# Kernel optimization log

Measured on AMD Instinct MI355X. Metric: run time of the kernel, lower is better.

## Reference

```python
import jax, jax.numpy as jnp
import numpy as np

N, E, IN, OUT = 50000, 1600000, 64, 64
DIM, K = 2, 5          # pseudo-coordinate dim, kernel size per dim
KP = K ** DIM          # 25 kernel weight matrices
S = 2 ** DIM           # 4 non-zero linear B-spline basis products per edge
# bit pattern per basis product: bits[s, d] in {0,1}
_BITS = np.array([[(s >> d) & 1 for d in range(DIM)] for s in range(S)], dtype=np.int32)
_OFFS = np.array([K ** (DIM - 1 - d) for d in range(DIM)], dtype=np.int32)  # row-major flatten


def setup_inputs() -> dict:
    key = jax.random.key(0)
    ks = jax.random.split(key, 6)
    x = jax.random.normal(ks[0], (N, IN), dtype=jnp.float32)
    edge_index = jax.random.randint(ks[1], (2, E), 0, N)
    pseudo = jax.random.uniform(ks[2], (E, DIM), dtype=jnp.float32)
    bnd = 1.0 / np.sqrt(KP * IN)  # matches uniform(size) init in reset_parameters
    weight = jax.random.uniform(ks[3], (KP, IN, OUT), dtype=jnp.float32, minval=-bnd, maxval=bnd)
    root_weight = jax.random.uniform(ks[4], (IN, OUT), dtype=jnp.float32, minval=-bnd, maxval=bnd)
    bias = jax.random.uniform(ks[5], (OUT,), dtype=jnp.float32, minval=-bnd, maxval=bnd)
    return {"x": x, "edge_index": edge_index, "pseudo": pseudo,
            "weight": weight, "root_weight": root_weight, "bias": bias}


def _basis_and_index(pseudo):
    # open B-spline, degree 1: scale by (K - 1)
    v = pseudo * jnp.asarray(K - 1, pseudo.dtype)          # [E, DIM]
    lo = jnp.floor(v)
    frac = v - lo                                          # [E, DIM]
    lo = lo.astype(jnp.int32)
    bits = jnp.asarray(_BITS)                              # [S, DIM]
    # basis[e, s] = prod_d (frac if bit else 1-frac)
    terms = jnp.where(bits[None].astype(bool), frac[:, None, :], 1.0 - frac[:, None, :])
    basis = jnp.prod(terms, axis=-1)                       # [E, S]
    idx_d = (lo[:, None, :] + bits[None]) % K              # [E, S, DIM]; wrap is harmless (basis=0 there)
    idx = jnp.sum(idx_d * jnp.asarray(_OFFS), axis=-1)     # [E, S] flat weight index in [0, KP)
    return basis, idx


def reference(x, edge_index, pseudo, weight, root_weight, bias):
    row, col = edge_index[0], edge_index[1]                # row = target, col = source
    basis, idx = _basis_and_index(pseudo)                  # [E,S], [E,S]
    x_src = x[col]                                         # [E, IN] gather
    # Accumulate basis-weighted source features per (target node, kernel index),
    # then apply the dense [KP, IN, OUT] weights once (same math, no [E,IN,OUT] blowup).
    acc = jnp.zeros((N * KP, IN), x.dtype)
    for s in range(S):  # S=4, fixed structural loop
        acc = acc + jax.ops.segment_sum(basis[:, s:s + 1] * x_src,
                                        row * KP + idx[:, s], num_segments=N * KP)
    out = jnp.einsum('nki,kio->no', acc.reshape(N, KP, IN), weight)  # [N, OUT]
    deg = jax.ops.segment_sum(jnp.ones((E,), x.dtype), row, num_segments=N)
    out = out / jnp.clip(deg, 1.0)[:, None]                # mean over neighbors (1/N(i))
    return out + x @ root_weight + bias
```

## Files before the change

kernel.cpp:

```cpp
#include <hip/hip_runtime.h>
#include <hip/hip_fp16.h>
#include <hip/hip_bf16.h>


#define NN    50000
#define EE    1600000
#define NPB   16
#define KD    1664
#define ASTB  1672
#define CAP   56
#define OFCAP 16384

#define REC_B 6250
#define XB_B  1563
#define WT_B  104

typedef unsigned short ushort_t;
typedef __attribute__((ext_vector_type(8))) short short8;
typedef __attribute__((ext_vector_type(4))) float f32x4;

static __device__ __forceinline__ ushort_t f2bf(float f) {
  union { float f; unsigned u; } v; v.f = f;
  return (ushort_t)((v.u + 0x7fffu + ((v.u >> 16) & 1u)) >> 16);
}
static __device__ __forceinline__ unsigned pk2bf(float a, float b) {
  __hip_bfloat162 h = __float22bfloat162_rn(make_float2(a, b));
  union { __hip_bfloat162 h; unsigned u; } cv; cv.h = h; return cv.u;
}
union S8 { short8 s; unsigned u[4]; };

__global__ __launch_bounds__(256) void k_prep(
    const int* __restrict__ ei, const float* __restrict__ pseudo,
    int* __restrict__ cursor, uint2* __restrict__ recs, uint4* __restrict__ ofl,
    const float* __restrict__ x, ushort_t* __restrict__ xb,
    const float* __restrict__ w, const float* __restrict__ root,
    ushort_t* __restrict__ wt, int useXB) {
  const int b = blockIdx.x;
  if (b < REC_B) {
    int e = b * 256 + threadIdx.x;
    int row = ei[e], col = ei[EE + e];
    float2 pv = ((const float2*)pseudo)[e];
    float v0 = pv.x * 4.0f, v1 = pv.y * 4.0f;
    int slot = atomicAdd(&cursor[row], 1);
    if (slot < CAP) {
      unsigned h0 = __half_as_ushort(__float2half(v0));
      unsigned h1 = __half_as_ushort(__float2half(v1));
      recs[row * CAP + slot] = make_uint2((unsigned)col, h0 | (h1 << 16));
    } else {
      int o = atomicAdd(&cursor[NN], 1);
      if (o < OFCAP)
        ofl[o] = make_uint4((unsigned)row, (unsigned)col,
                            __float_as_uint(v0), __float_as_uint(v1));
    }
  } else if (b < REC_B + XB_B) {
    if (!useXB) return;
    int t = (b - REC_B) * 256 + threadIdx.x;
    if (t < NN * 8) {
      const float4* xp = (const float4*)x + (size_t)t * 2;
      float4 aa = xp[0], bb = xp[1];
      S8 o;
      o.u[0] = pk2bf(aa.x, aa.y); o.u[1] = pk2bf(aa.z, aa.w);
      o.u[2] = pk2bf(bb.x, bb.y); o.u[3] = pk2bf(bb.z, bb.w);
      ((short8*)xb)[t] = o.s;
    }
  } else {
    int t = (b - REC_B - XB_B) * 256 + threadIdx.x;
    int idx = t * 4;
    if (idx < 64 * KD) {
      int o = idx / KD, k = idx - o * KD;
#pragma unroll
      for (int q = 0; q < 4; ++q) {
        int kk = k + q;
        wt[idx + q] = (kk < 1600) ? f2bf(w[kk * 64 + o]) : f2bf(root[(kk - 1600) * 64 + o]);
      }
    }
  }
}

template <bool XBF>
__global__ __launch_bounds__(1024) void k_main(
    const uint2* __restrict__ recs, const int* __restrict__ cursor,
    const uint4* __restrict__ ofl,
    const float* __restrict__ x, const ushort_t* __restrict__ xb,
    const ushort_t* __restrict__ wt, const float* __restrict__ bias,
    float* __restrict__ out) {
  __shared__ ushort_t accS[NPB * ASTB];
  __shared__ float    outp[4 * NPB * 64];
  __shared__ float    sinv[NPB];
  const int tid = threadIdx.x;
  const int lane = tid & 63;
  const int w = tid >> 6;
  const int nb = blockIdx.x * NPB;
  const int node = nb + w;

  const int dg = cursor[node];
  const int m = min(dg, CAP);
  const float dcf = (float)max(dg, 1);
  if (lane == 0) sinv[w] = 1.0f / dcf;
  accS[w * ASTB + 1600 + lane] = f2bf(x[(size_t)node * 64 + lane] * dcf);

  const int m15 = lane & 15, quad = lane >> 4;
  const float r0f = (float)(m15 / 5),        c0f = (float)(m15 % 5);
  const float r1f = (float)((16 + m15) / 5), c1f = (float)((16 + m15) % 5);

  f32x4 acc[2][4];
#pragma unroll
  for (int a = 0; a < 2; ++a)
#pragma unroll
    for (int b = 0; b < 4; ++b) acc[a][b] = (f32x4){0.f, 0.f, 0.f, 0.f};

  const uint2* bket = recs + (size_t)node * CAP;
  unsigned rcx = 0u, rcy = 0x7C007C00u;
  if (lane < m) { uint2 rr = bket[lane]; rcx = rr.x; rcy = rr.y; }

  for (int e0 = 0; e0 < m; e0 += 32) {
    const int eb = e0 + quad * 8;
    unsigned cj[8], pj[8];
#pragma unroll
    for (int j = 0; j < 8; ++j) {
      cj[j] = (unsigned)__shfl((int)rcx, eb + j);
      pj[j] = (unsigned)__shfl((int)rcy, eb + j);
    }
    S8 aT0, aT1, bT[4];
#pragma unroll
    for (int p = 0; p < 4; ++p) {
      if (XBF) {
        const ushort_t* xr0 = xb + (size_t)cj[2 * p] * 64 + m15;
        const ushort_t* xr1 = xb + (size_t)cj[2 * p + 1] * 64 + m15;
        unsigned l0 = xr0[0], l1 = xr0[16], l2 = xr0[32], l3 = xr0[48];
        unsigned h0 = xr1[0], h1 = xr1[16], h2 = xr1[32], h3 = xr1[48];
        bT[0].u[p] = l0 | (h0 << 16);
        bT[1].u[p] = l1 | (h1 << 16);
        bT[2].u[p] = l2 | (h2 << 16);
        bT[3].u[p] = l3 | (h3 << 16);
      } else {
        const float* xr0 = x + (size_t)cj[2 * p] * 64 + m15;
        const float* xr1 = x + (size_t)cj[2 * p + 1] * 64 + m15;
        bT[0].u[p] = pk2bf(xr0[0],  xr1[0]);
        bT[1].u[p] = pk2bf(xr0[16], xr1[16]);
        bT[2].u[p] = pk2bf(xr0[32], xr1[32]);
        bT[3].u[p] = pk2bf(xr0[48], xr1[48]);
      }
    }
#pragma unroll
    for (int p = 0; p < 4; ++p) {
      float a0[2], a1[2];
#pragma unroll
      for (int q = 0; q < 2; ++q) {
        unsigned pv = pj[2 * p + q];
        float v0 = __half2float(__ushort_as_half((ushort_t)(pv & 0xFFFFu)));
        float v1 = __half2float(__ushort_as_half((ushort_t)(pv >> 16)));
        a0[q] = fmaxf(0.f, 1.f - fabsf(v0 - r0f)) * fmaxf(0.f, 1.f - fabsf(v1 - c0f));
        a1[q] = fmaxf(0.f, 1.f - fabsf(v0 - r1f)) * fmaxf(0.f, 1.f - fabsf(v1 - c1f));
      }
      aT0.u[p] = pk2bf(a0[0], a0[1]);
      aT1.u[p] = pk2bf(a1[0], a1[1]);
    }
    __builtin_amdgcn_s_setprio(1);
#pragma unroll
    for (int t = 0; t < 4; ++t) {
      acc[0][t] = __builtin_amdgcn_mfma_f32_16x16x32_bf16(aT0.s, bT[t].s, acc[0][t], 0, 0, 0);
      acc[1][t] = __builtin_amdgcn_mfma_f32_16x16x32_bf16(aT1.s, bT[t].s, acc[1][t], 0, 0, 0);
    }
    __builtin_amdgcn_s_setprio(0);
  }

  {
    int ofc = min(cursor[NN], OFCAP);
    for (int i = 0; i < ofc; ++i) {
      uint4 r = ofl[i];
      if ((int)r.x != node) continue;
      float v0 = __uint_as_float(r.z), v1 = __uint_as_float(r.w);
      float h00 = fmaxf(0.f, 1.f - fabsf(v0 - r0f));
      float h01 = fmaxf(0.f, 1.f - fabsf(v1 - c0f));
      float h10 = fmaxf(0.f, 1.f - fabsf(v0 - r1f));
      float h11 = fmaxf(0.f, 1.f - fabsf(v1 - c1f));
      float mk = (quad == 0) ? 1.0f : 0.0f;
      S8 aT0, aT1, bT[4];
#pragma unroll
      for (int p = 0; p < 4; ++p) { aT0.u[p] = 0; aT1.u[p] = 0; }
      aT0.u[0] = pk2bf(h00 * h01 * mk, 0.0f);
      aT1.u[0] = pk2bf(h10 * h11 * mk, 0.0f);
      const float* xr = x + (size_t)r.y * 64 + m15;
#pragma unroll
      for (int t = 0; t < 4; ++t) {
        float xv = xr[16 * t];
#pragma unroll
        for (int p = 0; p < 4; ++p) bT[t].u[p] = pk2bf(xv, xv);
      }
#pragma unroll
      for (int t = 0; t < 4; ++t) {
        acc[0][t] = __builtin_amdgcn_mfma_f32_16x16x32_bf16(aT0.s, bT[t].s, acc[0][t], 0, 0, 0);
        acc[1][t] = __builtin_amdgcn_mfma_f32_16x16x32_bf16(aT1.s, bT[t].s, acc[1][t], 0, 0, 0);
      }
    }
  }

#pragma unroll
  for (int mt = 0; mt < 2; ++mt)
#pragma unroll
    for (int r = 0; r < 4; ++r) {
      int kp = mt * 16 + quad * 4 + r;
      if (kp < 25) {
#pragma unroll
        for (int nt = 0; nt < 4; ++nt)
          accS[w * ASTB + kp * 64 + nt * 16 + m15] = f2bf(acc[mt][nt][r]);
      }
    }
  __syncthreads();

  {
    const int ntile = w & 3, kh = w >> 2;
    const int m2 = lane & 15, quad2 = lane >> 4;
    const int nn2 = ntile * 16 + m2;
    f32x4 d = {0.0f, 0.0f, 0.0f, 0.0f};
    const ushort_t* ab = &accS[m2 * ASTB + kh * 416 + quad2 * 8];
    const ushort_t* wb = &wt[(size_t)nn2 * KD + kh * 416 + quad2 * 8];
    for (int kk = 0; kk < 13; ++kk) {
      short8 af = *(const short8*)(ab + kk * 32);
      short8 bf = *(const short8*)(wb + kk * 32);
      d = __builtin_amdgcn_mfma_f32_16x16x32_bf16(af, bf, d, 0, 0, 0);
    }
#pragma unroll
    for (int r = 0; r < 4; ++r)
      outp[kh * (NPB * 64) + (quad2 * 4 + r) * 64 + ntile * 16 + m2] = d[r];
  }
  __syncthreads();

  {
    float conv = outp[0 * (NPB * 64) + w * 64 + lane]
               + outp[1 * (NPB * 64) + w * 64 + lane]
               + outp[2 * (NPB * 64) + w * 64 + lane]
               + outp[3 * (NPB * 64) + w * 64 + lane];
    out[(size_t)node * 64 + lane] = conv * sinv[w] + bias[lane];
  }
}

__global__ void k_sentinel(float* __restrict__ out) {
  int i = blockIdx.x * 256 + threadIdx.x;
  if (i < NN * 64) out[i] = 1000.0f;
}

extern "C" void kernel_launch(void* const* d_in, const int* in_sizes, int n_in,
                              void* d_out, int out_size, void* d_ws, size_t ws_size,
                              hipStream_t stream) {
  const float* x      = (const float*)d_in[0];
  const int*   ei     = (const int*)d_in[1];
  const float* pseudo = (const float*)d_in[2];
  const float* w      = (const float*)d_in[3];
  const float* root   = (const float*)d_in[4];
  const float* bias   = (const float*)d_in[5];
  float* out = (float*)d_out;
  (void)in_sizes; (void)n_in; (void)out_size;

  char* ws = (char*)d_ws;
  size_t off = 0;
  auto alloc = [&](size_t bytes) { size_t r = off; off += (bytes + 511) & ~(size_t)511; return r; };
  ushort_t* wt     = (ushort_t*)(ws + alloc((size_t)64 * KD * 2));
  int*      cursor = (int*)(ws + alloc((size_t)(NN + 1) * 4));
  uint4*    ofl    = (uint4*)(ws + alloc((size_t)OFCAP * 16));
  uint2*    recs   = (uint2*)(ws + alloc((size_t)NN * CAP * 8));
  size_t baseNeed  = off;
  ushort_t* xb     = (ushort_t*)(ws + alloc((size_t)NN * 64 * 2));
  size_t fullNeed  = off;

  if (ws_size < baseNeed) {
    k_sentinel<<<(NN * 64 + 255) / 256, 256, 0, stream>>>(out);
    return;
  }
  const int useXB = (ws_size >= fullNeed) ? 1 : 0;

  hipMemsetAsync(cursor, 0, (size_t)(NN + 1) * 4, stream);
  k_prep<<<REC_B + XB_B + WT_B, 256, 0, stream>>>(ei, pseudo, cursor, recs, ofl,
                                                  x, xb, w, root, wt, useXB);
  if (useXB)
    k_main<true><<<NN / NPB, 1024, 0, stream>>>(recs, cursor, ofl, x, xb, wt, bias, out);
  else
    k_main<false><<<NN / NPB, 1024, 0, stream>>>(recs, cursor, ofl, x, xb, wt, bias, out);
}
```

Measured before the change: 352.8 us.

## Replace per-node fixed-capacity buckets with two-level coarse bucket sort into CSR

Edge binning now scatters records into sharded coarse buckets of 128 nodes using few, padded atomic counters. A new sort kernel counts and scans per-node degrees in shared memory and writes a compact CSR layout with per-node start and degree. The main kernel reads variable-length neighbour lists, reloading records every 64 edges, so the overflow list scan over all nodes is gone. Gathers are issued ahead of the basis arithmetic, and launch bounds request more occupancy. This costs an extra kernel launch and another pass over the edges, and coarse buckets that overflow their fixed capacity silently drop edges.

```diff
diff --git a/kernel.cpp b/kernel.cpp
--- a/kernel.cpp
+++ b/kernel.cpp
@@ -8,8 +8,11 @@
 #define NPB   16
 #define KD    1664
 #define ASTB  1672
-#define CAP   56
-#define OFCAP 16384
+
+#define NB    391
+#define NSH   4
+#define CCAP  1280
+#define CSTR  16
 
 #define REC_B 6250
 #define XB_B  1563
@@ -31,30 +34,27 @@
 
 __global__ __launch_bounds__(256) void k_prep(
     const int* __restrict__ ei, const float* __restrict__ pseudo,
-    int* __restrict__ cursor, uint2* __restrict__ recs, uint4* __restrict__ ofl,
+    int* __restrict__ ccur, uint2* __restrict__ coarse,
     const float* __restrict__ x, ushort_t* __restrict__ xb,
     const float* __restrict__ w, const float* __restrict__ root,
     ushort_t* __restrict__ wt, int useXB) {
   const int b = blockIdx.x;
+  const int tid = threadIdx.x;
   if (b < REC_B) {
-    int e = b * 256 + threadIdx.x;
+    int e = b * 256 + tid;
     int row = ei[e], col = ei[EE + e];
     float2 pv = ((const float2*)pseudo)[e];
     float v0 = pv.x * 4.0f, v1 = pv.y * 4.0f;
-    int slot = atomicAdd(&cursor[row], 1);
-    if (slot < CAP) {
-      unsigned h0 = __half_as_ushort(__float2half(v0));
-      unsigned h1 = __half_as_ushort(__float2half(v1));
-      recs[row * CAP + slot] = make_uint2((unsigned)col, h0 | (h1 << 16));
-    } else {
-      int o = atomicAdd(&cursor[NN], 1);
-      if (o < OFCAP)
-        ofl[o] = make_uint4((unsigned)row, (unsigned)col,
-                            __float_as_uint(v0), __float_as_uint(v1));
-    }
+    unsigned h0 = __half_as_ushort(__float2half(v0));
+    unsigned h1 = __half_as_ushort(__float2half(v1));
+    int c4 = (row >> 7) * NSH + (tid & (NSH - 1));
+    int slot = atomicAdd(&ccur[c4 * CSTR], 1);
+    if (slot < CCAP)
+      coarse[(size_t)c4 * CCAP + slot] =
+          make_uint2((unsigned)col | ((unsigned)(row & 127) << 16), h0 | (h1 << 16));
   } else if (b < REC_B + XB_B) {
     if (!useXB) return;
-    int t = (b - REC_B) * 256 + threadIdx.x;
+    int t = (b - REC_B) * 256 + tid;
     if (t < NN * 8) {
       const float4* xp = (const float4*)x + (size_t)t * 2;
       float4 aa = xp[0], bb = xp[1];
@@ -64,7 +64,7 @@
       ((short8*)xb)[t] = o.s;
     }
   } else {
-    int t = (b - REC_B - XB_B) * 256 + threadIdx.x;
+    int t = (b - REC_B - XB_B) * 256 + tid;
     int idx = t * 4;
     if (idx < 64 * KD) {
       int o = idx / KD, k = idx - o * KD;
@@ -77,10 +77,56 @@
   }
 }
 
+__global__ __launch_bounds__(256) void k_sort(
+    const int* __restrict__ ccur, const uint2* __restrict__ coarse,
+    uint2* __restrict__ recs, int* __restrict__ startA, int* __restrict__ degA) {
+  __shared__ int cnt[128], lpos[128], scn[128], red[256];
+  const int c = blockIdx.x, tid = threadIdx.x;
+  if (tid < 128) cnt[tid] = 0;
+  const int pc = c * NSH;
+  int a = 0;
+  for (int i = tid; i < pc; i += 256) a += min(ccur[i * CSTR], CCAP);
+  red[tid] = a;
+  __syncthreads();
+  for (int s = 128; s > 0; s >>= 1) { if (tid < s) red[tid] += red[tid + s]; __syncthreads(); }
+  const int base = red[0];
+  for (int s = 0; s < NSH; ++s) {
+    int n = min(ccur[(pc + s) * CSTR], CCAP);
+    const uint2* seg = coarse + (size_t)(pc + s) * CCAP;
+    for (int i = tid; i < n; i += 256) atomicAdd(&cnt[(seg[i].x >> 16) & 127], 1);
+  }
+  __syncthreads();
+  if (tid < 128) scn[tid] = cnt[tid];
+  __syncthreads();
+  for (int ofs = 1; ofs < 128; ofs <<= 1) {
+    int v = 0;
+    if (tid < 128 && tid >= ofs) v = scn[tid - ofs];
+    __syncthreads();
+    if (tid < 128 && tid >= ofs) scn[tid] += v;
+    __syncthreads();
+  }
+  if (tid < 128) {
+    int excl = scn[tid] - cnt[tid];
+    lpos[tid] = base + excl;
+    int row = c * 128 + tid;
+    if (row < NN) { startA[row] = base + excl; degA[row] = cnt[tid]; }
+  }
+  __syncthreads();
+  for (int s = 0; s < NSH; ++s) {
+    int n = min(ccur[(pc + s) * CSTR], CCAP);
+    const uint2* seg = coarse + (size_t)(pc + s) * CCAP;
+    for (int i = tid; i < n; i += 256) {
+      uint2 r = seg[i];
+      int dst = atomicAdd(&lpos[(r.x >> 16) & 127], 1);
+      recs[dst] = make_uint2(r.x & 0xFFFFu, r.y);
+    }
+  }
+}
+
 template <bool XBF>
-__global__ __launch_bounds__(1024) void k_main(
-    const uint2* __restrict__ recs, const int* __restrict__ cursor,
-    const uint4* __restrict__ ofl,
+__global__ __launch_bounds__(1024, 4) void k_main(
+    const uint2* __restrict__ recs, const int* __restrict__ startA,
+    const int* __restrict__ degA,
     const float* __restrict__ x, const ushort_t* __restrict__ xb,
     const ushort_t* __restrict__ wt, const float* __restrict__ bias,
     float* __restrict__ out) {
@@ -90,12 +136,10 @@
   const int tid = threadIdx.x;
   const int lane = tid & 63;
   const int w = tid >> 6;
-  const int nb = blockIdx.x * NPB;
-  const int node = nb + w;
-
-  const int dg = cursor[node];
-  const int m = min(dg, CAP);
-  const float dcf = (float)max(dg, 1);
+  const int node = blockIdx.x * NPB + w;
+
+  const int m = degA[node];
+  const float dcf = (float)max(m, 1);
   if (lane == 0) sinv[w] = 1.0f / dcf;
   accS[w * ASTB + 1600 + lane] = f2bf(x[(size_t)node * 64 + lane] * dcf);
 
@@ -109,39 +153,36 @@
 #pragma unroll
     for (int b = 0; b < 4; ++b) acc[a][b] = (f32x4){0.f, 0.f, 0.f, 0.f};
 
-  const uint2* bket = recs + (size_t)node * CAP;
+  const uint2* bket = recs + startA[node];
   unsigned rcx = 0u, rcy = 0x7C007C00u;
   if (lane < m) { uint2 rr = bket[lane]; rcx = rr.x; rcy = rr.y; }
 
   for (int e0 = 0; e0 < m; e0 += 32) {
-    const int eb = e0 + quad * 8;
+    if (e0 && !(e0 & 63)) {
+      rcx = 0u; rcy = 0x7C007C00u;
+      int idx = e0 + lane;
+      if (idx < m) { uint2 rr = bket[idx]; rcx = rr.x; rcy = rr.y; }
+    }
+    const int eb = (e0 & 32) + quad * 8;
     unsigned cj[8], pj[8];
 #pragma unroll
     for (int j = 0; j < 8; ++j) {
       cj[j] = (unsigned)__shfl((int)rcx, eb + j);
       pj[j] = (unsigned)__shfl((int)rcy, eb + j);
     }
+    unsigned gv[4][8];
+    float    gf[4][8];
+#pragma unroll
+    for (int j = 0; j < 8; ++j) {
+      if (XBF) {
+        const ushort_t* xr = xb + (size_t)cj[j] * 64 + m15;
+        gv[0][j] = xr[0]; gv[1][j] = xr[16]; gv[2][j] = xr[32]; gv[3][j] = xr[48];
+      } else {
+        const float* xr = x + (size_t)cj[j] * 64 + m15;
+        gf[0][j] = xr[0]; gf[1][j] = xr[16]; gf[2][j] = xr[32]; gf[3][j] = xr[48];
+      }
+    }
     S8 aT0, aT1, bT[4];
-#pragma unroll
-    for (int p = 0; p < 4; ++p) {
-      if (XBF) {
-        const ushort_t* xr0 = xb + (size_t)cj[2 * p] * 64 + m15;
-        const ushort_t* xr1 = xb + (size_t)cj[2 * p + 1] * 64 + m15;
-        unsigned l0 = xr0[0], l1 = xr0[16], l2 = xr0[32], l3 = xr0[48];
-        unsigned h0 = xr1[0], h1 = xr1[16], h2 = xr1[32], h3 = xr1[48];
-        bT[0].u[p] = l0 | (h0 << 16);
-        bT[1].u[p] = l1 | (h1 << 16);
-        bT[2].u[p] = l2 | (h2 << 16);
-        bT[3].u[p] = l3 | (h3 << 16);
-      } else {
-        const float* xr0 = x + (size_t)cj[2 * p] * 64 + m15;
-        const float* xr1 = x + (size_t)cj[2 * p + 1] * 64 + m15;
-        bT[0].u[p] = pk2bf(xr0[0],  xr1[0]);
-        bT[1].u[p] = pk2bf(xr0[16], xr1[16]);
-        bT[2].u[p] = pk2bf(xr0[32], xr1[32]);
-        bT[3].u[p] = pk2bf(xr0[48], xr1[48]);
-      }
-    }
 #pragma unroll
     for (int p = 0; p < 4; ++p) {
       float a0[2], a1[2];
@@ -156,6 +197,12 @@
       aT0.u[p] = pk2bf(a0[0], a0[1]);
       aT1.u[p] = pk2bf(a1[0], a1[1]);
     }
+#pragma unroll
+    for (int p = 0; p < 4; ++p)
+#pragma unroll
+      for (int t = 0; t < 4; ++t)
+        bT[t].u[p] = XBF ? (gv[t][2 * p] | (gv[t][2 * p + 1] << 16))
+                         : pk2bf(gf[t][2 * p], gf[t][2 * p + 1]);
     __builtin_amdgcn_s_setprio(1);
 #pragma unroll
     for (int t = 0; t < 4; ++t) {
@@ -163,37 +210,6 @@
       acc[1][t] = __builtin_amdgcn_mfma_f32_16x16x32_bf16(aT1.s, bT[t].s, acc[1][t], 0, 0, 0);
     }
     __builtin_amdgcn_s_setprio(0);
-  }
-
-  {
-    int ofc = min(cursor[NN], OFCAP);
-    for (int i = 0; i < ofc; ++i) {
-      uint4 r = ofl[i];
-      if ((int)r.x != node) continue;
-      float v0 = __uint_as_float(r.z), v1 = __uint_as_float(r.w);
-      float h00 = fmaxf(0.f, 1.f - fabsf(v0 - r0f));
-      float h01 = fmaxf(0.f, 1.f - fabsf(v1 - c0f));
-      float h10 = fmaxf(0.f, 1.f - fabsf(v0 - r1f));
-      float h11 = fmaxf(0.f, 1.f - fabsf(v1 - c1f));
-      float mk = (quad == 0) ? 1.0f : 0.0f;
-      S8 aT0, aT1, bT[4];
-#pragma unroll
-      for (int p = 0; p < 4; ++p) { aT0.u[p] = 0; aT1.u[p] = 0; }
-      aT0.u[0] = pk2bf(h00 * h01 * mk, 0.0f);
-      aT1.u[0] = pk2bf(h10 * h11 * mk, 0.0f);
-      const float* xr = x + (size_t)r.y * 64 + m15;
-#pragma unroll
-      for (int t = 0; t < 4; ++t) {
-        float xv = xr[16 * t];
-#pragma unroll
-        for (int p = 0; p < 4; ++p) bT[t].u[p] = pk2bf(xv, xv);
-      }
-#pragma unroll
-      for (int t = 0; t < 4; ++t) {
-        acc[0][t] = __builtin_amdgcn_mfma_f32_16x16x32_bf16(aT0.s, bT[t].s, acc[0][t], 0, 0, 0);
-        acc[1][t] = __builtin_amdgcn_mfma_f32_16x16x32_bf16(aT1.s, bT[t].s, acc[1][t], 0, 0, 0);
-      }
-    }
   }
 
 #pragma unroll
@@ -257,9 +273,11 @@
   size_t off = 0;
   auto alloc = [&](size_t bytes) { size_t r = off; off += (bytes + 511) & ~(size_t)511; return r; };
   ushort_t* wt     = (ushort_t*)(ws + alloc((size_t)64 * KD * 2));
-  int*      cursor = (int*)(ws + alloc((size_t)(NN + 1) * 4));
-  uint4*    ofl    = (uint4*)(ws + alloc((size_t)OFCAP * 16));
-  uint2*    recs   = (uint2*)(ws + alloc((size_t)NN * CAP * 8));
+  int*      ccur   = (int*)(ws + alloc((size_t)NB * NSH * CSTR * 4));
+  int*      startA = (int*)(ws + alloc((size_t)NN * 4));
+  int*      degA   = (int*)(ws + alloc((size_t)NN * 4));
+  uint2*    recs   = (uint2*)(ws + alloc((size_t)EE * 8));
+  uint2*    coarse = (uint2*)(ws + alloc((size_t)NB * NSH * CCAP * 8));
   size_t baseNeed  = off;
   ushort_t* xb     = (ushort_t*)(ws + alloc((size_t)NN * 64 * 2));
   size_t fullNeed  = off;
@@ -270,11 +288,12 @@
   }
   const int useXB = (ws_size >= fullNeed) ? 1 : 0;
 
-  hipMemsetAsync(cursor, 0, (size_t)(NN + 1) * 4, stream);
-  k_prep<<<REC_B + XB_B + WT_B, 256, 0, stream>>>(ei, pseudo, cursor, recs, ofl,
+  hipMemsetAsync(ccur, 0, (size_t)NB * NSH * CSTR * 4, stream);
+  k_prep<<<REC_B + XB_B + WT_B, 256, 0, stream>>>(ei, pseudo, ccur, coarse,
                                                   x, xb, w, root, wt, useXB);
+  k_sort<<<NB, 256, 0, stream>>>(ccur, coarse, recs, startA, degA);
   if (useXB)
-    k_main<true><<<NN / NPB, 1024, 0, stream>>>(recs, cursor, ofl, x, xb, wt, bias, out);
+    k_main<true><<<NN / NPB, 1024, 0, stream>>>(recs, startA, degA, x, xb, wt, bias, out);
   else
-    k_main<false><<<NN / NPB, 1024, 0, stream>>>(recs, cursor, ofl, x, xb, wt, bias, out);
-}
+    k_main<false><<<NN / NPB, 1024, 0, stream>>>(recs, startA, degA, x, xb, wt, bias, out);
+}
```

Measured after the change: 325.7 us. -7.7%, faster.
